# Performance work log

Hardware: AMD Instinct MI355X
Metric: run time of the kernel (lower is better)

Reference implementation:

```python
import jax, jax.numpy as jnp
import numpy as np

HIDDEN = 2048
INTER = 1408
N_ROUTED = 32
N_SHARED = 2
TOP_K = 6
B, S = 2, 1024


def setup_inputs() -> dict:
    key = jax.random.key(0)
    ks = jax.random.split(key, 9)
    scale = 0.02
    x = jax.random.normal(ks[0], (B, S, HIDDEN), dtype=jnp.float32)
    w_router = jax.random.normal(ks[1], (HIDDEN, N_ROUTED), dtype=jnp.float32) * scale
    wg = jax.random.normal(ks[2], (N_ROUTED, HIDDEN, INTER), dtype=jnp.float32) * scale
    wu = jax.random.normal(ks[3], (N_ROUTED, HIDDEN, INTER), dtype=jnp.float32) * scale
    wd = jax.random.normal(ks[4], (N_ROUTED, INTER, HIDDEN), dtype=jnp.float32) * scale
    sg = jax.random.normal(ks[5], (N_SHARED, HIDDEN, INTER), dtype=jnp.float32) * scale
    su = jax.random.normal(ks[6], (N_SHARED, HIDDEN, INTER), dtype=jnp.float32) * scale
    sd = jax.random.normal(ks[7], (N_SHARED, INTER, HIDDEN), dtype=jnp.float32) * scale
    return {"x": x, "w_router": w_router, "wg": wg, "wu": wu, "wd": wd,
            "sg": sg, "su": su, "sd": sd}


def _swiglu(xf, wg_e, wu_e, wd_e):
    # xf: [T, D]; wg_e/wu_e: [D, F]; wd_e: [F, D]
    h = jax.nn.silu(xf @ wg_e) * (xf @ wu_e)
    return h @ wd_e


def reference(x, w_router, wg, wu, wd, sg, su, sd):
    Bb, Ss, D = x.shape
    xf = x.reshape(-1, D)                      # [T, D], T = B*S
    T = xf.shape[0]

    # Shared experts: applied densely to every token, summed.
    shared = jnp.zeros_like(xf)
    for i in range(sg.shape[0]):               # small fixed count (2)
        shared = shared + _swiglu(xf, sg[i], su[i], sd[i])

    # Router: softmax over all routed experts, then top-k + renormalize.
    probs = jax.nn.softmax(xf @ w_router, axis=-1)            # [T, E]
    topw, topi = jax.lax.top_k(probs, TOP_K)                  # [T, K]
    topw = topw / jnp.sum(topw, axis=-1, keepdims=True)

    # Dense [T, E] combine weights (zero where expert not selected).
    E = wg.shape[0]
    wdense = jnp.zeros((T, E), dtype=xf.dtype)
    wdense = wdense.at[jnp.arange(T)[:, None], topi].add(topw)

    # Scan over experts, accumulating weighted expert outputs (memory-light).
    def body(acc, ew):
        wg_e, wu_e, wd_e, w_e = ew            # w_e: [T] combine weight for this expert
        y = _swiglu(xf, wg_e, wu_e, wd_e)     # [T, D]
        return acc + w_e[:, None] * y, None

    routed, _ = jax.lax.scan(body, jnp.zeros_like(xf), (wg, wu, wd, wdense.T))

    return (shared + routed).reshape(Bb, Ss, D)
```

## Files before the change

### kernel.cpp

```cpp
#include <hip/hip_runtime.h>
#include <hip/hip_bf16.h>

#define T_TOK 2048
#define D_HID 2048
#define F_INT 1408
#define N_EXP 32
#define TOPK 6
#define NJOBS 34
#define SH_BASE 12288
#define ROWS_TOTAL 16384
#define BM 128
#define MAXTILES 160
#define LDSW 40

typedef __bf16 bf16;
typedef __bf16 bf16x4 __attribute__((ext_vector_type(4)));
typedef __bf16 bf16x8 __attribute__((ext_vector_type(8)));
typedef float f32x4 __attribute__((ext_vector_type(4)));

__device__ __forceinline__ int swz(int r, int k) {
    return r * LDSW + (((k >> 2) ^ ((r >> 2) & 7)) << 2) + (k & 3);
}

__global__ __launch_bounds__(256) void k_router(const float* __restrict__ x,
                                                const float* __restrict__ wr,
                                                int* __restrict__ counts,
                                                int* __restrict__ tok_e,
                                                float* __restrict__ tok_w) {
    int t = blockIdx.x;
    int tid = threadIdx.x;
    __shared__ float xs[D_HID];
    __shared__ float part[8][32];
    __shared__ float probs[N_EXP];

    const float4* xsrc = (const float4*)(x + (size_t)t * D_HID);
    float4* xdst = (float4*)xs;
    for (int i = tid; i < D_HID / 4; i += 256) xdst[i] = xsrc[i];
    __syncthreads();

    int e = tid & 31, c = tid >> 5;
    float p = 0.f;
    const float* wp = wr + e;
    #pragma unroll 8
    for (int h = c * 256; h < c * 256 + 256; ++h) p += xs[h] * wp[h * 32];
    part[c][e] = p;
    __syncthreads();

    if (tid < 32) {
        float l = 0.f;
        #pragma unroll
        for (int cc = 0; cc < 8; ++cc) l += part[cc][tid];
        float m = l;
        for (int off = 16; off; off >>= 1) m = fmaxf(m, __shfl_xor(m, off));
        float ex = __expf(l - m);
        float s = ex;
        for (int off = 16; off; off >>= 1) s += __shfl_xor(s, off);
        probs[tid] = ex / s;
    }
    __syncthreads();

    if (tid == 0) {
        unsigned used = 0;
        int ids[TOPK]; float wsv[TOPK]; float wsum = 0.f;
        for (int k = 0; k < TOPK; ++k) {
            int best = 0; float bv = -1.f;
            for (int ee = 0; ee < N_EXP; ++ee)
                if (!((used >> ee) & 1u) && probs[ee] > bv) { bv = probs[ee]; best = ee; }
            used |= 1u << best;
            ids[k] = best; wsv[k] = bv; wsum += bv;
        }
        float inv = 1.f / wsum;
        for (int k = 0; k < TOPK; ++k) {
            tok_e[t * TOPK + k] = ids[k];
            tok_w[t * TOPK + k] = wsv[k] * inv;
            atomicAdd(&counts[ids[k]], 1);
        }
    }
}

__global__ void k_plan(const int* __restrict__ counts, int* __restrict__ offs,
                       int* __restrict__ cursors, int* __restrict__ tile_job,
                       int* __restrict__ tile_m0, int* __restrict__ ntiles) {
    int tid = threadIdx.x;
    if (tid < N_EXP) cursors[tid] = 0;
    if (tid == 0) {
        int o = 0;
        offs[0] = 0;
        for (int e2 = 0; e2 < N_EXP; ++e2) { o += counts[e2]; offs[e2 + 1] = o; }
        offs[33] = offs[32] + T_TOK;
        offs[34] = offs[33] + T_TOK;
        int nt = 0;
        for (int j = 0; j < NJOBS; ++j) {
            int cnt = (j < N_EXP) ? counts[j] : T_TOK;
            for (int m0 = 0; m0 < cnt; m0 += BM) { tile_job[nt] = j; tile_m0[nt] = m0; ++nt; }
        }
        *ntiles = nt;
    }
}

__global__ __launch_bounds__(256) void k_assign(const int* __restrict__ tok_e,
                                                const int* __restrict__ offs,
                                                int* __restrict__ cursors,
                                                int* __restrict__ slots,
                                                int* __restrict__ rowtok) {
    int t = blockIdx.x * 256 + threadIdx.x;
    #pragma unroll
    for (int k = 0; k < TOPK; ++k) {
        int e = tok_e[t * TOPK + k];
        int pos = atomicAdd(&cursors[e], 1);
        int slot = offs[e] + pos;
        slots[t * TOPK + k] = slot;
        rowtok[slot] = t;
    }
    rowtok[SH_BASE + t] = t;
    rowtok[SH_BASE + T_TOK + t] = t;
}

__global__ __launch_bounds__(256, 2) void k_gateup(
    const float* __restrict__ x, const float* __restrict__ wg, const float* __restrict__ wu,
    const float* __restrict__ sg, const float* __restrict__ su,
    const int* __restrict__ rowtok, const int* __restrict__ counts, const int* __restrict__ offs,
    const int* __restrict__ tile_job, const int* __restrict__ tile_m0,
    const int* __restrict__ ntiles, bf16* __restrict__ H) {

    int ty = blockIdx.y;
    if (ty >= *ntiles) return;
    int job = tile_job[ty];
    int m0 = tile_m0[ty];
    int cnt = (job < N_EXP) ? counts[job] : T_TOK;
    int base = offs[job];
    int n0 = blockIdx.x * 128;
    const float* Wg = (job < N_EXP) ? wg + (size_t)job * D_HID * F_INT
                                    : sg + (size_t)(job - N_EXP) * D_HID * F_INT;
    const float* Wu = (job < N_EXP) ? wu + (size_t)job * D_HID * F_INT
                                    : su + (size_t)(job - N_EXP) * D_HID * F_INT;

    __shared__ bf16 As[128 * LDSW];
    __shared__ bf16 Bg[128 * LDSW];
    __shared__ bf16 Bu[128 * LDSW];

    int tid = threadIdx.x;
    int lane = tid & 63;
    int wid = tid >> 6;
    int wm = (wid >> 1) * 64;
    int wn = (wid & 1) * 64;

    int ar = tid >> 1;
    int akh = (tid & 1) * 16;
    int grow_a = m0 + ar; if (grow_a > cnt - 1) grow_a = cnt - 1;
    const float* asrc = x + (size_t)rowtok[base + grow_a] * D_HID + akh;

    int k4 = (tid >> 5) * 4;
    int nn = (tid & 31) * 4;
    const float* gsrc = Wg + (size_t)k4 * F_INT + n0 + nn;
    const float* usrc = Wu + (size_t)k4 * F_INT + n0 + nn;

    f32x4 accg[4][4], accu[4][4];
    f32x4 zero = {0.f, 0.f, 0.f, 0.f};
    #pragma unroll
    for (int i = 0; i < 4; ++i)
        #pragma unroll
        for (int j = 0; j < 4; ++j) { accg[i][j] = zero; accu[i][j] = zero; }

    float4 a_r[4], g_r[4], u_r[4];

    auto LOAD = [&](int k0) {
        const float4* s4 = (const float4*)(asrc + k0);
        a_r[0] = s4[0]; a_r[1] = s4[1]; a_r[2] = s4[2]; a_r[3] = s4[3];
        const float* g0 = gsrc + (size_t)k0 * F_INT;
        g_r[0] = *(const float4*)g0;
        g_r[1] = *(const float4*)(g0 + F_INT);
        g_r[2] = *(const float4*)(g0 + 2 * F_INT);
        g_r[3] = *(const float4*)(g0 + 3 * F_INT);
        const float* u0 = usrc + (size_t)k0 * F_INT;
        u_r[0] = *(const float4*)u0;
        u_r[1] = *(const float4*)(u0 + F_INT);
        u_r[2] = *(const float4*)(u0 + 2 * F_INT);
        u_r[3] = *(const float4*)(u0 + 3 * F_INT);
    };

    auto WRITE = [&]() {
        #pragma unroll
        for (int q = 0; q < 4; ++q) {
            float4 f = a_r[q];
            bf16x4 v = {(bf16)f.x, (bf16)f.y, (bf16)f.z, (bf16)f.w};
            *(bf16x4*)&As[swz(ar, akh + 4 * q)] = v;
        }
        bf16x4 p0 = {(bf16)g_r[0].x, (bf16)g_r[1].x, (bf16)g_r[2].x, (bf16)g_r[3].x};
        bf16x4 p1 = {(bf16)g_r[0].y, (bf16)g_r[1].y, (bf16)g_r[2].y, (bf16)g_r[3].y};
        bf16x4 p2 = {(bf16)g_r[0].z, (bf16)g_r[1].z, (bf16)g_r[2].z, (bf16)g_r[3].z};
        bf16x4 p3 = {(bf16)g_r[0].w, (bf16)g_r[1].w, (bf16)g_r[2].w, (bf16)g_r[3].w};
        *(bf16x4*)&Bg[swz(nn + 0, k4)] = p0;
        *(bf16x4*)&Bg[swz(nn + 1, k4)] = p1;
        *(bf16x4*)&Bg[swz(nn + 2, k4)] = p2;
        *(bf16x4*)&Bg[swz(nn + 3, k4)] = p3;
        bf16x4 q0 = {(bf16)u_r[0].x, (bf16)u_r[1].x, (bf16)u_r[2].x, (bf16)u_r[3].x};
        bf16x4 q1 = {(bf16)u_r[0].y, (bf16)u_r[1].y, (bf16)u_r[2].y, (bf16)u_r[3].y};
        bf16x4 q2 = {(bf16)u_r[0].z, (bf16)u_r[1].z, (bf16)u_r[2].z, (bf16)u_r[3].z};
        bf16x4 q3 = {(bf16)u_r[0].w, (bf16)u_r[1].w, (bf16)u_r[2].w, (bf16)u_r[3].w};
        *(bf16x4*)&Bu[swz(nn + 0, k4)] = q0;
        *(bf16x4*)&Bu[swz(nn + 1, k4)] = q1;
        *(bf16x4*)&Bu[swz(nn + 2, k4)] = q2;
        *(bf16x4*)&Bu[swz(nn + 3, k4)] = q3;
    };

    const int NT = D_HID / 32;
    LOAD(0);
    for (int kt = 0; kt < NT; ++kt) {
        WRITE();
        __syncthreads();
        if (kt + 1 < NT) LOAD((kt + 1) * 32);

        int kk = (lane >> 4) * 8;
        bf16x8 af[4];
        #pragma unroll
        for (int mf = 0; mf < 4; ++mf) {
            int R = wm + mf * 16 + (lane & 15);
            bf16x4 lo = *(const bf16x4*)&As[swz(R, kk)];
            bf16x4 hi = *(const bf16x4*)&As[swz(R, kk + 4)];
            af[mf] = __builtin_shufflevector(lo, hi, 0, 1, 2, 3, 4, 5, 6, 7);
        }
        #pragma unroll
        for (int nf = 0; nf < 4; ++nf) {
            int rn = wn + nf * 16 + (lane & 15);
            int o0 = swz(rn, kk), o1 = swz(rn, kk + 4);
            bf16x4 bl = *(const bf16x4*)&Bg[o0];
            bf16x4 bh = *(const bf16x4*)&Bg[o1];
            bf16x8 bfr = __builtin_shufflevector(bl, bh, 0, 1, 2, 3, 4, 5, 6, 7);
            bf16x4 ul = *(const bf16x4*)&Bu[o0];
            bf16x4 uh = *(const bf16x4*)&Bu[o1];
            bf16x8 ufr = __builtin_shufflevector(ul, uh, 0, 1, 2, 3, 4, 5, 6, 7);
            #pragma unroll
            for (int mf = 0; mf < 4; ++mf) {
                accg[mf][nf] = __builtin_amdgcn_mfma_f32_16x16x32_bf16(af[mf], bfr, accg[mf][nf], 0, 0, 0);
                accu[mf][nf] = __builtin_amdgcn_mfma_f32_16x16x32_bf16(af[mf], ufr, accu[mf][nf], 0, 0, 0);
            }
        }
        asm volatile("s_barrier" ::: "memory");
    }

    #pragma unroll
    for (int mf = 0; mf < 4; ++mf) {
        #pragma unroll
        for (int nf = 0; nf < 4; ++nf) {
            int col = n0 + wn + nf * 16 + (lane & 15);
            #pragma unroll
            for (int r = 0; r < 4; ++r) {
                int grow = m0 + wm + mf * 16 + (lane >> 4) * 4 + r;
                if (grow < cnt) {
                    float g = accg[mf][nf][r];
                    float u = accu[mf][nf][r];
                    float h = g * u / (1.f + __expf(-g));
                    H[(size_t)(base + grow) * F_INT + col] = (bf16)h;
                }
            }
        }
    }
}

__global__ __launch_bounds__(256, 2) void k_down(
    const bf16* __restrict__ H, const float* __restrict__ wd, const float* __restrict__ sd,
    const int* __restrict__ counts, const int* __restrict__ offs,
    const int* __restrict__ tile_job, const int* __restrict__ tile_m0,
    const int* __restrict__ ntiles, bf16* __restrict__ P) {

    int ty = blockIdx.y;
    if (ty >= *ntiles) return;
    int job = tile_job[ty];
    int m0 = tile_m0[ty];
    int cnt = (job < N_EXP) ? counts[job] : T_TOK;
    int base = offs[job];
    int n0 = blockIdx.x * 128;
    const float* Wd = (job < N_EXP) ? wd + (size_t)job * F_INT * D_HID
                                    : sd + (size_t)(job - N_EXP) * F_INT * D_HID;

    __shared__ bf16 As[128 * LDSW];
    __shared__ bf16 Bs[128 * LDSW];

    int tid = threadIdx.x;
    int lane = tid & 63;
    int wid = tid >> 6;
    int wm = (wid >> 1) * 64;
    int wn = (wid & 1) * 64;

    int ar = tid >> 1;
    int akh = (tid & 1) * 16;
    int grow_a = m0 + ar; if (grow_a > cnt - 1) grow_a = cnt - 1;
    const bf16* asrc = H + (size_t)(base + grow_a) * F_INT + akh;

    int k4 = (tid >> 5) * 4;
    int nn = (tid & 31) * 4;
    const float* bsrc = Wd + (size_t)k4 * D_HID + n0 + nn;

    f32x4 acc[4][4];
    f32x4 zero = {0.f, 0.f, 0.f, 0.f};
    #pragma unroll
    for (int i = 0; i < 4; ++i)
        #pragma unroll
        for (int j = 0; j < 4; ++j) acc[i][j] = zero;

    bf16x8 h_r[2];
    float4 b_r[4];

    auto LOAD = [&](int k0) {
        h_r[0] = *(const bf16x8*)(asrc + k0);
        h_r[1] = *(const bf16x8*)(asrc + k0 + 8);
        const float* b0 = bsrc + (size_t)k0 * D_HID;
        b_r[0] = *(const float4*)b0;
        b_r[1] = *(const float4*)(b0 + D_HID);
        b_r[2] = *(const float4*)(b0 + 2 * D_HID);
        b_r[3] = *(const float4*)(b0 + 3 * D_HID);
    };

    auto WRITE = [&]() {
        bf16x4 w0 = __builtin_shufflevector(h_r[0], h_r[0], 0, 1, 2, 3);
        bf16x4 w1 = __builtin_shufflevector(h_r[0], h_r[0], 4, 5, 6, 7);
        bf16x4 w2 = __builtin_shufflevector(h_r[1], h_r[1], 0, 1, 2, 3);
        bf16x4 w3 = __builtin_shufflevector(h_r[1], h_r[1], 4, 5, 6, 7);
        *(bf16x4*)&As[swz(ar, akh + 0)]  = w0;
        *(bf16x4*)&As[swz(ar, akh + 4)]  = w1;
        *(bf16x4*)&As[swz(ar, akh + 8)]  = w2;
        *(bf16x4*)&As[swz(ar, akh + 12)] = w3;
        bf16x4 p0 = {(bf16)b_r[0].x, (bf16)b_r[1].x, (bf16)b_r[2].x, (bf16)b_r[3].x};
        bf16x4 p1 = {(bf16)b_r[0].y, (bf16)b_r[1].y, (bf16)b_r[2].y, (bf16)b_r[3].y};
        bf16x4 p2 = {(bf16)b_r[0].z, (bf16)b_r[1].z, (bf16)b_r[2].z, (bf16)b_r[3].z};
        bf16x4 p3 = {(bf16)b_r[0].w, (bf16)b_r[1].w, (bf16)b_r[2].w, (bf16)b_r[3].w};
        *(bf16x4*)&Bs[swz(nn + 0, k4)] = p0;
        *(bf16x4*)&Bs[swz(nn + 1, k4)] = p1;
        *(bf16x4*)&Bs[swz(nn + 2, k4)] = p2;
        *(bf16x4*)&Bs[swz(nn + 3, k4)] = p3;
    };

    const int NT = F_INT / 32;
    LOAD(0);
    for (int kt = 0; kt < NT; ++kt) {
        WRITE();
        __syncthreads();
        if (kt + 1 < NT) LOAD((kt + 1) * 32);

        int kk = (lane >> 4) * 8;
        bf16x8 af[4];
        #pragma unroll
        for (int mf = 0; mf < 4; ++mf) {
            int R = wm + mf * 16 + (lane & 15);
            bf16x4 lo = *(const bf16x4*)&As[swz(R, kk)];
            bf16x4 hi = *(const bf16x4*)&As[swz(R, kk + 4)];
            af[mf] = __builtin_shufflevector(lo, hi, 0, 1, 2, 3, 4, 5, 6, 7);
        }
        #pragma unroll
        for (int nf = 0; nf < 4; ++nf) {
            int rn = wn + nf * 16 + (lane & 15);
            bf16x4 bl = *(const bf16x4*)&Bs[swz(rn, kk)];
            bf16x4 bh = *(const bf16x4*)&Bs[swz(rn, kk + 4)];
            bf16x8 bfr = __builtin_shufflevector(bl, bh, 0, 1, 2, 3, 4, 5, 6, 7);
            #pragma unroll
            for (int mf = 0; mf < 4; ++mf)
                acc[mf][nf] = __builtin_amdgcn_mfma_f32_16x16x32_bf16(af[mf], bfr, acc[mf][nf], 0, 0, 0);
        }
        asm volatile("s_barrier" ::: "memory");
    }

    #pragma unroll
    for (int mf = 0; mf < 4; ++mf) {
        #pragma unroll
        for (int nf = 0; nf < 4; ++nf) {
            int col = n0 + wn + nf * 16 + (lane & 15);
            #pragma unroll
            for (int r = 0; r < 4; ++r) {
                int grow = m0 + wm + mf * 16 + (lane >> 4) * 4 + r;
                if (grow < cnt)
                    P[(size_t)(base + grow) * D_HID + col] = (bf16)acc[mf][nf][r];
            }
        }
    }
}

__global__ __launch_bounds__(256) void k_combine(const bf16* __restrict__ P,
                                                 const int* __restrict__ slots,
                                                 const float* __restrict__ tok_w,
                                                 float* __restrict__ out) {
    int t = blockIdx.x;
    int tid = threadIdx.x;
    __shared__ int ss[TOPK];
    __shared__ float ww[TOPK];
    if (tid < TOPK) { ss[tid] = slots[t * TOPK + tid]; ww[tid] = tok_w[t * TOPK + tid]; }
    __syncthreads();
    int c0 = tid * 8;
    float acc[8];
    {
        bf16x8 v0 = *(const bf16x8*)(P + (size_t)(SH_BASE + t) * D_HID + c0);
        bf16x8 v1 = *(const bf16x8*)(P + (size_t)(SH_BASE + T_TOK + t) * D_HID + c0);
        #pragma unroll
        for (int i = 0; i < 8; ++i) acc[i] = (float)v0[i] + (float)v1[i];
    }
    #pragma unroll
    for (int k = 0; k < TOPK; ++k) {
        bf16x8 v = *(const bf16x8*)(P + (size_t)ss[k] * D_HID + c0);
        float w = ww[k];
        #pragma unroll
        for (int i = 0; i < 8; ++i) acc[i] += w * (float)v[i];
    }
    float4 o0 = {acc[0], acc[1], acc[2], acc[3]};
    float4 o1 = {acc[4], acc[5], acc[6], acc[7]};
    *(float4*)(out + (size_t)t * D_HID + c0) = o0;
    *(float4*)(out + (size_t)t * D_HID + c0 + 4) = o1;
}

extern "C" void kernel_launch(void* const* d_in, const int* in_sizes, int n_in,
                              void* d_out, int out_size, void* d_ws, size_t ws_size,
                              hipStream_t stream) {
    const float* x  = (const float*)d_in[0];
    const float* wr = (const float*)d_in[1];
    const float* wg = (const float*)d_in[2];
    const float* wu = (const float*)d_in[3];
    const float* wd = (const float*)d_in[4];
    const float* sg = (const float*)d_in[5];
    const float* su = (const float*)d_in[6];
    const float* sd = (const float*)d_in[7];
    float* out = (float*)d_out;

    char* w = (char*)d_ws;
    int*   counts   = (int*)(w + 0);
    int*   cursors  = (int*)(w + 256);
    int*   offs     = (int*)(w + 512);
    int*   ntiles   = (int*)(w + 1024);
    int*   tile_job = (int*)(w + 2048);
    int*   tile_m0  = (int*)(w + 4096);
    int*   tok_e    = (int*)(w + 8192);
    float* tok_w    = (float*)(w + 8192 + 49152);
    int*   slots    = (int*)(w + 8192 + 2 * 49152);
    int*   rowtok   = (int*)(w + 8192 + 3 * 49152);
    bf16*  H        = (bf16*)(w + 262144);
    bf16*  P        = (bf16*)(w + 262144 + (size_t)ROWS_TOTAL * F_INT * 2);

    hipMemsetAsync(counts, 0, 128, stream);
    k_router<<<T_TOK, 256, 0, stream>>>(x, wr, counts, tok_e, tok_w);
    k_plan<<<1, 64, 0, stream>>>(counts, offs, cursors, tile_job, tile_m0, ntiles);
    k_assign<<<T_TOK / 256, 256, 0, stream>>>(tok_e, offs, cursors, slots, rowtok);
    k_gateup<<<dim3(F_INT / 128, MAXTILES), 256, 0, stream>>>(
        x, wg, wu, sg, su, rowtok, counts, offs, tile_job, tile_m0, ntiles, H);
    k_down<<<dim3(D_HID / 128, MAXTILES), 256, 0, stream>>>(
        H, wd, sd, counts, offs, tile_job, tile_m0, ntiles, P);
    k_combine<<<T_TOK, 256, 0, stream>>>(P, slots, tok_w, out);
}
```

Baseline: 921.7 us.

## Decode MoE tiles on device with XCD-aware 1D grid ordering

Removes the precomputed tile table and has each block decode its (job, n0, m0) tile from the expert counts using a flattened 1D grid. The linear index is remapped so that blocks assigned to the same XCD (bid mod 8) process contiguous ranges of tiles, grouping tiles of the same expert and weight column for better L2 reuse. Adds a small per-block loop over the counts in exchange for fewer global lookups and a leaner planning kernel.

```diff
diff --git a/kernel.cpp b/kernel.cpp
--- a/kernel.cpp
+++ b/kernel.cpp
@@ -10,7 +10,7 @@
 #define SH_BASE 12288
 #define ROWS_TOTAL 16384
 #define BM 128
-#define MAXTILES 160
+#define MAXT 159
 #define LDSW 40
 
 typedef __bf16 bf16;
@@ -20,6 +20,34 @@
 
 __device__ __forceinline__ int swz(int r, int k) {
     return r * LDSW + (((k >> 2) ^ ((r >> 2) & 7)) << 2) + (k & 3);
+}
+
+__device__ __forceinline__ int decode_tile(const int* __restrict__ counts, int bid, int NBN,
+                                           int& job, int& n0, int& m0) {
+    int total = 0;
+    for (int j = 0; j < NJOBS; ++j) {
+        int c = (j < N_EXP) ? counts[j] : T_TOK;
+        total += ((c + BM - 1) >> 7) * NBN;
+    }
+    if (bid >= total) return 0;
+    int q = total >> 3, r = total & 7, x = bid & 7, o = bid >> 3;
+    int L = (x < r ? x * (q + 1) : r * (q + 1) + (x - r) * q) + o;
+    int acc = 0;
+    for (int j = 0; j < NJOBS; ++j) {
+        int c = (j < N_EXP) ? counts[j] : T_TOK;
+        int tc = (c + BM - 1) >> 7;
+        int b = tc * NBN;
+        if (L < acc + b) {
+            int rem = L - acc;
+            int n0i = rem / tc;
+            job = j;
+            n0 = n0i << 7;
+            m0 = (rem - n0i * tc) << 7;
+            return 1;
+        }
+        acc += b;
+    }
+    return 0;
 }
 
 __global__ __launch_bounds__(256) void k_router(const float* __restrict__ x,
@@ -79,8 +107,7 @@
 }
 
 __global__ void k_plan(const int* __restrict__ counts, int* __restrict__ offs,
-                       int* __restrict__ cursors, int* __restrict__ tile_job,
-                       int* __restrict__ tile_m0, int* __restrict__ ntiles) {
+                       int* __restrict__ cursors) {
     int tid = threadIdx.x;
     if (tid < N_EXP) cursors[tid] = 0;
     if (tid == 0) {
@@ -89,12 +116,6 @@
         for (int e2 = 0; e2 < N_EXP; ++e2) { o += counts[e2]; offs[e2 + 1] = o; }
         offs[33] = offs[32] + T_TOK;
         offs[34] = offs[33] + T_TOK;
-        int nt = 0;
-        for (int j = 0; j < NJOBS; ++j) {
-            int cnt = (j < N_EXP) ? counts[j] : T_TOK;
-            for (int m0 = 0; m0 < cnt; m0 += BM) { tile_job[nt] = j; tile_m0[nt] = m0; ++nt; }
-        }
-        *ntiles = nt;
     }
 }
 
@@ -120,16 +141,12 @@
     const float* __restrict__ x, const float* __restrict__ wg, const float* __restrict__ wu,
     const float* __restrict__ sg, const float* __restrict__ su,
     const int* __restrict__ rowtok, const int* __restrict__ counts, const int* __restrict__ offs,
-    const int* __restrict__ tile_job, const int* __restrict__ tile_m0,
-    const int* __restrict__ ntiles, bf16* __restrict__ H) {
-
-    int ty = blockIdx.y;
-    if (ty >= *ntiles) return;
-    int job = tile_job[ty];
-    int m0 = tile_m0[ty];
+    bf16* __restrict__ H) {
+
+    int job, n0, m0;
+    if (!decode_tile(counts, blockIdx.x, F_INT / 128, job, n0, m0)) return;
     int cnt = (job < N_EXP) ? counts[job] : T_TOK;
     int base = offs[job];
-    int n0 = blockIdx.x * 128;
     const float* Wg = (job < N_EXP) ? wg + (size_t)job * D_HID * F_INT
                                     : sg + (size_t)(job - N_EXP) * D_HID * F_INT;
     const float* Wu = (job < N_EXP) ? wu + (size_t)job * D_HID * F_INT
@@ -261,16 +278,12 @@
 __global__ __launch_bounds__(256, 2) void k_down(
     const bf16* __restrict__ H, const float* __restrict__ wd, const float* __restrict__ sd,
     const int* __restrict__ counts, const int* __restrict__ offs,
-    const int* __restrict__ tile_job, const int* __restrict__ tile_m0,
-    const int* __restrict__ ntiles, bf16* __restrict__ P) {
-
-    int ty = blockIdx.y;
-    if (ty >= *ntiles) return;
-    int job = tile_job[ty];
-    int m0 = tile_m0[ty];
+    bf16* __restrict__ P) {
+
+    int job, n0, m0;
+    if (!decode_tile(counts, blockIdx.x, D_HID / 128, job, n0, m0)) return;
     int cnt = (job < N_EXP) ? counts[job] : T_TOK;
     int base = offs[job];
-    int n0 = blockIdx.x * 128;
     const float* Wd = (job < N_EXP) ? wd + (size_t)job * F_INT * D_HID
                                     : sd + (size_t)(job - N_EXP) * F_INT * D_HID;
 
@@ -423,9 +436,6 @@
     int*   counts   = (int*)(w + 0);
     int*   cursors  = (int*)(w + 256);
     int*   offs     = (int*)(w + 512);
-    int*   ntiles   = (int*)(w + 1024);
-    int*   tile_job = (int*)(w + 2048);
-    int*   tile_m0  = (int*)(w + 4096);
     int*   tok_e    = (int*)(w + 8192);
     float* tok_w    = (float*)(w + 8192 + 49152);
     int*   slots    = (int*)(w + 8192 + 2 * 49152);
@@ -435,11 +445,11 @@
 
     hipMemsetAsync(counts, 0, 128, stream);
     k_router<<<T_TOK, 256, 0, stream>>>(x, wr, counts, tok_e, tok_w);
-    k_plan<<<1, 64, 0, stream>>>(counts, offs, cursors, tile_job, tile_m0, ntiles);
+    k_plan<<<1, 64, 0, stream>>>(counts, offs, cursors);
     k_assign<<<T_TOK / 256, 256, 0, stream>>>(tok_e, offs, cursors, slots, rowtok);
-    k_gateup<<<dim3(F_INT / 128, MAXTILES), 256, 0, stream>>>(
-        x, wg, wu, sg, su, rowtok, counts, offs, tile_job, tile_m0, ntiles, H);
-    k_down<<<dim3(D_HID / 128, MAXTILES), 256, 0, stream>>>(
-        H, wd, sd, counts, offs, tile_job, tile_m0, ntiles, P);
+    k_gateup<<<MAXT * (F_INT / 128), 256, 0, stream>>>(
+        x, wg, wu, sg, su, rowtok, counts, offs, H);
+    k_down<<<MAXT * (D_HID / 128), 256, 0, stream>>>(
+        H, wd, sd, counts, offs, P);
     k_combine<<<T_TOK, 256, 0, stream>>>(P, slots, tok_w, out);
 }
```

Result: faster. 854.1 us (-7.3%).
